# Kernel tuning notes

Hardware: AMD Instinct MI355X
Metric: run time of the kernel (lower is better)

## Reference

```python
import jax, jax.numpy as jnp
import numpy as np

EMBED_DIM = 1024
N_HEADS = 16
HEAD_DIM = EMBED_DIM // N_HEADS


def setup_inputs() -> dict:
    key = jax.random.key(0)
    k_x, k_wqkv, k_bqkv, k_wo, k_bo = jax.random.split(key, 5)
    s = 1.0 / np.sqrt(EMBED_DIM)
    return {
        "x": jax.random.normal(k_x, (2, 2048, EMBED_DIM), dtype=jnp.float32),
        "w_qkv": jax.random.uniform(k_wqkv, (EMBED_DIM, 3 * EMBED_DIM), jnp.float32, -s, s),
        "b_qkv": jax.random.uniform(k_bqkv, (3 * EMBED_DIM,), jnp.float32, -s, s),
        "w_out": jax.random.uniform(k_wo, (EMBED_DIM, EMBED_DIM), jnp.float32, -s, s),
        "b_out": jax.random.uniform(k_bo, (EMBED_DIM,), jnp.float32, -s, s),
    }


def reference(x, w_qkv, b_qkv, w_out, b_out):
    B, T, C = x.shape
    qkv = x @ w_qkv + b_qkv                      # [B,T,3C]
    q, k, v = jnp.split(qkv, 3, axis=-1)
    # [B,T,C] -> [B,H,T,D]
    def heads(t):
        return t.reshape(B, T, N_HEADS, HEAD_DIM).transpose(0, 2, 1, 3)
    q, k, v = heads(q), heads(k), heads(v)
    scale = 1.0 / np.sqrt(HEAD_DIM).astype(np.float32)
    scores = jnp.einsum("bhqd,bhkd->bhqk", q, k) * scale
    causal = jnp.tril(jnp.ones((T, T), dtype=bool))  # True where allowed
    scores = jnp.where(causal, scores, jnp.finfo(scores.dtype).min)
    attn = jax.nn.softmax(scores, axis=-1)
    out = jnp.einsum("bhqk,bhkd->bhqd", attn, v)
    out = out.transpose(0, 2, 1, 3).reshape(B, T, C)
    return out @ w_out + b_out
```

## Files before the change

kernel.cpp:

```cpp
#include <hip/hip_runtime.h>
#include <hip/hip_bf16.h>

typedef __attribute__((ext_vector_type(4))) float f32x4;
typedef __attribute__((ext_vector_type(8))) short bf16x8;

static __device__ __forceinline__ unsigned short f2bf(float f) {
  union { float f; unsigned u; } v;
  v.f = f;
  unsigned r = v.u + 0x7FFFu + ((v.u >> 16) & 1u);
  return (unsigned short)(r >> 16);
}

static __device__ __forceinline__ unsigned cvt_pk_bf16(float lo, float hi) {
  unsigned r;
  asm("v_cvt_pk_bf16_f32 %0, %1, %2" : "=v"(r) : "v"(lo), "v"(hi));
  return r;
}

static __device__ __forceinline__ void gload16(const void* g, void* lds) {
  __builtin_amdgcn_global_load_lds(
      (const __attribute__((address_space(1))) unsigned int*)g,
      (__attribute__((address_space(3))) unsigned int*)lds, 16, 0, 0);
}

__global__ __launch_bounds__(256) void prep_kernel(
    const float* __restrict__ x, const float* __restrict__ w_qkv,
    const float* __restrict__ w_out, unsigned short* __restrict__ xb,
    unsigned short* __restrict__ wqkvT, unsigned short* __restrict__ woT) {
  __shared__ float tile[32][33];
  const int bid = blockIdx.x, tid = threadIdx.x;
  if (bid < 4096) {
    int i = bid * 256 + tid;
    float4 v = reinterpret_cast<const float4*>(x)[i];
    ushort4 o;
    o.x = f2bf(v.x); o.y = f2bf(v.y); o.z = f2bf(v.z); o.w = f2bf(v.w);
    reinterpret_cast<ushort4*>(xb)[i] = o;
    return;
  }
  const float* src; unsigned short* dst; int c0, r0, C;
  if (bid < 7168) {
    int t = bid - 4096;
    src = w_qkv; dst = wqkvT; C = 3072;
    c0 = (t % 96) * 32; r0 = (t / 96) * 32;
  } else {
    int t = bid - 7168;
    src = w_out; dst = woT; C = 1024;
    c0 = (t & 31) * 32; r0 = (t >> 5) * 32;
  }
  int tx = tid & 31, ty = tid >> 5;
#pragma unroll
  for (int i = 0; i < 32; i += 8)
    tile[ty + i][tx] = src[(size_t)(r0 + ty + i) * C + c0 + tx];
  __syncthreads();
#pragma unroll
  for (int i = 0; i < 32; i += 8)
    dst[(size_t)(c0 + ty + i) * 1024 + r0 + tx] = f2bf(tile[tx][ty + i]);
}

template <int MODE, int BN>
__global__ __launch_bounds__(256, MODE == 0 ? 3 : 2) void gemm_bf16(
    const unsigned short* __restrict__ A,
    const unsigned short* __restrict__ Bt,
    const float* __restrict__ bias,
    unsigned short* __restrict__ q_out,
    unsigned short* __restrict__ k_out,
    unsigned short* __restrict__ v_out,
    float* __restrict__ f_out) {
  constexpr int NB2 = BN / 32;
  constexpr int NBL = BN / 64;
  __shared__ __align__(16) unsigned short As[2][128 * 32];
  __shared__ __align__(16) unsigned short Bs[2][BN * 32];

  const int tid = threadIdx.x;
  const int wid = tid >> 6, lane = tid & 63;
  const int l15 = lane & 15, g = lane >> 4;
  const int wm = wid >> 1, wn = wid & 1;
  const int n0 = blockIdx.x * BN, m0 = blockIdx.y * 128;

  f32x4 acc[4][NB2] = {};

  auto stage = [&](int k0, int bsel) {
#pragma unroll
    for (int i = 0; i < 2; ++i) {
      int t = tid + i * 256;
      int row = t >> 2, c8 = (t & 3) << 3;
      gload16(A + (size_t)(m0 + row) * 1024 + k0 + c8, &As[bsel][(i * 256 + wid * 64) * 8]);
    }
#pragma unroll
    for (int i = 0; i < NBL; ++i) {
      int t = tid + i * 256;
      int row = t >> 2, c8 = (t & 3) << 3;
      gload16(Bt + (size_t)(n0 + row) * 1024 + k0 + c8, &Bs[bsel][(i * 256 + wid * 64) * 8]);
    }
  };

  stage(0, 0);
  __syncthreads();
  for (int ks = 0; ks < 32; ++ks) {
    const int cur = ks & 1;
    if (ks + 1 < 32) stage((ks + 1) * 32, cur ^ 1);
    bf16x8 a[4], b[NB2];
#pragma unroll
    for (int mi = 0; mi < 4; ++mi)
      a[mi] = *reinterpret_cast<const bf16x8*>(&As[cur][(wm * 64 + mi * 16 + l15) * 32 + g * 8]);
#pragma unroll
    for (int ni = 0; ni < NB2; ++ni)
      b[ni] = *reinterpret_cast<const bf16x8*>(&Bs[cur][(wn * (BN / 2) + ni * 16 + l15) * 32 + g * 8]);
    __builtin_amdgcn_s_setprio(1);
#pragma unroll
    for (int mi = 0; mi < 4; ++mi)
#pragma unroll
      for (int ni = 0; ni < NB2; ++ni)
        acc[mi][ni] = __builtin_amdgcn_mfma_f32_16x16x32_bf16(a[mi], b[ni], acc[mi][ni], 0, 0, 0);
    __builtin_amdgcn_s_setprio(0);
    __syncthreads();
  }

  if (MODE == 0) {
    const int which = n0 >> 10;
    unsigned short* dst = (which == 0) ? q_out : (which == 1) ? k_out : v_out;
    const float oscale = (which == 0) ? 0.125f * 1.44269504f : 1.0f;
#pragma unroll
    for (int ni = 0; ni < NB2; ++ni) {
      int col = n0 + wn * (BN / 2) + ni * 16 + l15;
      int c = col & 1023;
      int h = c >> 6, d = c & 63;
      float bv = bias[col];
#pragma unroll
      for (int mi = 0; mi < 4; ++mi) {
#pragma unroll
        for (int r = 0; r < 4; ++r) {
          int rowg = m0 + wm * 64 + mi * 16 + g * 4 + r;
          int bb = rowg >> 11, tt = rowg & 2047;
          dst[((bb * 16 + h) * 2048 + tt) * 64 + d] = f2bf((acc[mi][ni][r] + bv) * oscale);
        }
      }
    }
  } else {
#pragma unroll
    for (int ni = 0; ni < NB2; ++ni) {
      int col = n0 + wn * (BN / 2) + ni * 16 + l15;
      float bv = bias[col];
#pragma unroll
      for (int mi = 0; mi < 4; ++mi)
#pragma unroll
        for (int r = 0; r < 4; ++r) {
          int rowg = m0 + wm * 64 + mi * 16 + g * 4 + r;
          f_out[(size_t)rowg * 1024 + col] = acc[mi][ni][r] + bv;
        }
    }
  }
}

#define KS_SZ (64 * 64)
#define VT_SZ (64 * 72)

__device__ __forceinline__ void attn_stage_K(const unsigned short* __restrict__ Kb,
                                             int k0, unsigned short* KsBuf,
                                             int tid, int wid) {
#pragma unroll
  for (int i = 0; i < 2; ++i) {
    int t = tid + i * 256;
    int row = t >> 3;
    int cb = (t & 7) << 4;
    int src = cb ^ ((row & 7) << 4);
    gload16((const char*)Kb + (size_t)(k0 + row) * 128 + src,
            (char*)KsBuf + (i * 256 + wid * 64) * 16);
  }
}

__device__ __forceinline__ void write_vt(unsigned short* VtBuf, int kvL, int d8,
                                         uint4 v0, uint4 v1) {
  unsigned* base = reinterpret_cast<unsigned*>(&VtBuf[(size_t)d8 * 72 + kvL]);
  unsigned lo, hi;
  lo = __builtin_amdgcn_perm(v1.x, v0.x, 0x05040100u);
  hi = __builtin_amdgcn_perm(v1.x, v0.x, 0x07060302u);
  base[0] = lo;   base[36] = hi;
  lo = __builtin_amdgcn_perm(v1.y, v0.y, 0x05040100u);
  hi = __builtin_amdgcn_perm(v1.y, v0.y, 0x07060302u);
  base[72] = lo;  base[108] = hi;
  lo = __builtin_amdgcn_perm(v1.z, v0.z, 0x05040100u);
  hi = __builtin_amdgcn_perm(v1.z, v0.z, 0x07060302u);
  base[144] = lo; base[180] = hi;
  lo = __builtin_amdgcn_perm(v1.w, v0.w, 0x05040100u);
  hi = __builtin_amdgcn_perm(v1.w, v0.w, 0x07060302u);
  base[216] = lo; base[252] = hi;
}

__device__ __forceinline__ void attn_run_qtile(
    const unsigned short* __restrict__ Qb,
    const unsigned short* __restrict__ Kb,
    const unsigned short* __restrict__ Vb,
    unsigned short* __restrict__ O,
    int b, int h, int q0, int nt,
    unsigned short* Ks, unsigned short* Vt, unsigned short* Ps,
    int tid, int wid, int l15, int g) {
  bf16x8 qf[2];
  {
    const unsigned short* qrow_p = Qb + (size_t)(q0 + wid * 16 + l15) * 64;
    qf[0] = *reinterpret_cast<const bf16x8*>(qrow_p + g * 8);
    qf[1] = *reinterpret_cast<const bf16x8*>(qrow_p + 32 + g * 8);
  }

  float m_run = -1e30f;
  float l_run = 0.0f;
  f32x4 ot[4] = {};
  const int qg = q0 + wid * 16 + l15;
  const int kvL = (tid & 31) * 2, d8 = (tid >> 5) * 8;
  const int qrow = wid * 16 + l15;

  attn_stage_K(Kb, 0, Ks, tid, wid);
  {
    const uint4* vp = reinterpret_cast<const uint4*>(Vb + (size_t)kvL * 64 + d8);
    write_vt(Vt, kvL, d8, vp[0], vp[8]);
  }
  __syncthreads();

  for (int t = 0; t < nt; ++t) {
    const unsigned short* KsC = Ks + (t & 1) * KS_SZ;
    const unsigned short* VtC = Vt + (t & 1) * VT_SZ;
    uint4 va, vb;
    const bool pf = (t + 1 < nt);
    if (pf) {
      attn_stage_K(Kb, (t + 1) << 6, Ks + ((t + 1) & 1) * KS_SZ, tid, wid);
      const uint4* vp = reinterpret_cast<const uint4*>(
          Vb + (size_t)(((t + 1) << 6) + kvL) * 64 + d8);
      va = vp[0];
      vb = vp[8];
    }

    f32x4 s[4] = {};
    __builtin_amdgcn_s_setprio(1);
#pragma unroll
    for (int kk = 0; kk < 2; ++kk)
#pragma unroll
      for (int mi = 0; mi < 4; ++mi) {
        int row = mi * 16 + l15;
        int cb = (kk * 64 + g * 16) ^ ((row & 7) << 4);
        bf16x8 kf = *reinterpret_cast<const bf16x8*>((const char*)KsC + row * 128 + cb);
        s[mi] = __builtin_amdgcn_mfma_f32_16x16x32_bf16(kf, qf[kk], s[mi], 0, 0, 0);
      }
    __builtin_amdgcn_s_setprio(0);

    if (t == nt - 1) {
      const int k0 = t << 6;
#pragma unroll
      for (int mi = 0; mi < 4; ++mi)
#pragma unroll
        for (int r = 0; r < 4; ++r) {
          int kvg = k0 + mi * 16 + g * 4 + r;
          s[mi][r] = (kvg <= qg) ? s[mi][r] : -1e30f;
        }
    }

    float pmax = -1e30f;
#pragma unroll
    for (int mi = 0; mi < 4; ++mi)
#pragma unroll
      for (int r = 0; r < 4; ++r) pmax = fmaxf(pmax, s[mi][r]);

    if (!__all(pmax <= m_run + 8.0f)) {
      float tmax = fmaxf(pmax, __shfl_xor(pmax, 16));
      tmax = fmaxf(tmax, __shfl_xor(tmax, 32));
      float m_new = fmaxf(m_run, tmax);
      float corr = __builtin_amdgcn_exp2f(m_run - m_new);
      l_run *= corr;
#pragma unroll
      for (int mi = 0; mi < 4; ++mi)
#pragma unroll
        for (int r = 0; r < 4; ++r) ot[mi][r] *= corr;
      m_run = m_new;
    }

    float tsum = 0.f;
#pragma unroll
    for (int mi = 0; mi < 4; ++mi) {
      float p0 = __builtin_amdgcn_exp2f(s[mi][0] - m_run);
      float p1 = __builtin_amdgcn_exp2f(s[mi][1] - m_run);
      float p2 = __builtin_amdgcn_exp2f(s[mi][2] - m_run);
      float p3 = __builtin_amdgcn_exp2f(s[mi][3] - m_run);
      tsum += (p0 + p1) + (p2 + p3);
      uint2 pk;
      pk.x = cvt_pk_bf16(p0, p1);
      pk.y = cvt_pk_bf16(p2, p3);
      *reinterpret_cast<uint2*>((char*)Ps + qrow * 144 + mi * 32 + g * 8) = pk;
    }
    l_run += tsum;

    __builtin_amdgcn_s_setprio(1);
#pragma unroll
    for (int kk = 0; kk < 2; ++kk) {
      bf16x8 pfr = *reinterpret_cast<const bf16x8*>(Ps + qrow * 72 + kk * 32 + g * 8);
#pragma unroll
      for (int mi = 0; mi < 4; ++mi) {
        bf16x8 vf = *reinterpret_cast<const bf16x8*>(VtC + (mi * 16 + l15) * 72 + kk * 32 + g * 8);
        ot[mi] = __builtin_amdgcn_mfma_f32_16x16x32_bf16(vf, pfr, ot[mi], 0, 0, 0);
      }
    }
    __builtin_amdgcn_s_setprio(0);

    if (pf) write_vt(Vt + ((t + 1) & 1) * VT_SZ, kvL, d8, va, vb);
    __syncthreads();
  }

  float l_tot = l_run + __shfl_xor(l_run, 16);
  l_tot += __shfl_xor(l_tot, 32);
  float inv_l = 1.0f / l_tot;

#pragma unroll
  for (int mi = 0; mi < 4; ++mi) {
    uint2 pk;
    pk.x = cvt_pk_bf16(ot[mi][0] * inv_l, ot[mi][1] * inv_l);
    pk.y = cvt_pk_bf16(ot[mi][2] * inv_l, ot[mi][3] * inv_l);
    int b0 = (mi * 32 + g * 8) ^ ((qrow & 7) << 4);
    *reinterpret_cast<uint2*>((char*)Ks + qrow * 128 + b0) = pk;
  }
  __syncthreads();
#pragma unroll
  for (int i = 0; i < 2; ++i) {
    int t = tid + i * 256;
    int row = t >> 3;
    int cb = (t & 7) << 4;
    int sw = cb ^ ((row & 7) << 4);
    bf16x8 vv = *reinterpret_cast<const bf16x8*>((const char*)Ks + row * 128 + sw);
    *reinterpret_cast<bf16x8*>(O + ((size_t)(b * 2048 + q0 + row)) * 1024 + h * 64 + (cb >> 1)) = vv;
  }
  __syncthreads();
}

__global__ __launch_bounds__(256, 2) void attn_fwd(
    const unsigned short* __restrict__ Q,
    const unsigned short* __restrict__ K,
    const unsigned short* __restrict__ V,
    unsigned short* __restrict__ O) {
  __shared__ __align__(16) unsigned short Ks[2 * KS_SZ];
  __shared__ __align__(16) unsigned short Vt[2 * VT_SZ];
  __shared__ __align__(16) unsigned short Ps[64 * 72];

  const int tid = threadIdx.x;
  const int wid = tid >> 6;
  const int l15 = tid & 15;
  const int g = (tid & 63) >> 4;

  int lin = blockIdx.x + (blockIdx.y << 4);
  int w = ((lin & 7) << 6) + (lin >> 3);
  const int pi = w & 15, bh = w >> 4;
  const int b = bh >> 4, h = bh & 15;

  const unsigned short* Qb = Q + (size_t)bh * 2048 * 64;
  const unsigned short* Kb = K + (size_t)bh * 2048 * 64;
  const unsigned short* Vb = V + (size_t)bh * 2048 * 64;

  attn_run_qtile(Qb, Kb, Vb, O, b, h, pi << 6, pi + 1, Ks, Vt, Ps, tid, wid, l15, g);
  attn_run_qtile(Qb, Kb, Vb, O, b, h, (31 - pi) << 6, 32 - pi, Ks, Vt, Ps, tid, wid, l15, g);
}

extern "C" void kernel_launch(void* const* d_in, const int* in_sizes, int n_in,
                              void* d_out, int out_size, void* d_ws, size_t ws_size,
                              hipStream_t stream) {
  const float* x = (const float*)d_in[0];
  const float* w_qkv = (const float*)d_in[1];
  const float* b_qkv = (const float*)d_in[2];
  const float* w_out = (const float*)d_in[3];
  const float* b_out = (const float*)d_in[4];
  float* out = (float*)d_out;
  char* ws = (char*)d_ws;

  unsigned short* xb    = (unsigned short*)d_out;
  unsigned short* wqkvT = (unsigned short*)(ws);
  unsigned short* woT   = (unsigned short*)(ws + 6291456);
  unsigned short* q_buf = (unsigned short*)(ws + 8388608);
  unsigned short* k_buf = (unsigned short*)(ws + 16777216);
  unsigned short* v_buf = (unsigned short*)(ws + 25165824);
  unsigned short* aout  = (unsigned short*)(ws + 33554432);

  prep_kernel<<<dim3(8192), dim3(256), 0, stream>>>(x, w_qkv, w_out, xb, wqkvT, woT);

  gemm_bf16<0, 128><<<dim3(24, 32), dim3(256), 0, stream>>>(
      xb, wqkvT, b_qkv, q_buf, k_buf, v_buf, nullptr);

  attn_fwd<<<dim3(16, 32), dim3(256), 0, stream>>>(q_buf, k_buf, v_buf, aout);

  gemm_bf16<1, 64><<<dim3(16, 32), dim3(256), 0, stream>>>(
      aout, woT, b_out, nullptr, nullptr, nullptr, out);
}
```

Measured before the change: 107.0 us.

## Process paired causal query tiles together in one KV pass

The attention kernel now runs both paired query tiles (short tile pi and long tile 31-pi) in a single loop over KV tiles. Each staged K/V tile is loaded once and shared by both, instead of the short tile's KV range being streamed twice. K and V fragments are hoisted into registers and reused by both MFMA chains, and the P buffer is doubled. The block-index mapping also changes to a 1D grid ordered by pair index. This raises register and LDS pressure and may reduce occupancy.

Result: no change. 108.6 us (+1.5%).

```diff
diff --git a/kernel.cpp b/kernel.cpp
--- a/kernel.cpp
+++ b/kernel.cpp
@@ -187,147 +187,6 @@
   base[216] = lo; base[252] = hi;
 }
 
-__device__ __forceinline__ void attn_run_qtile(
-    const unsigned short* __restrict__ Qb,
-    const unsigned short* __restrict__ Kb,
-    const unsigned short* __restrict__ Vb,
-    unsigned short* __restrict__ O,
-    int b, int h, int q0, int nt,
-    unsigned short* Ks, unsigned short* Vt, unsigned short* Ps,
-    int tid, int wid, int l15, int g) {
-  bf16x8 qf[2];
-  {
-    const unsigned short* qrow_p = Qb + (size_t)(q0 + wid * 16 + l15) * 64;
-    qf[0] = *reinterpret_cast<const bf16x8*>(qrow_p + g * 8);
-    qf[1] = *reinterpret_cast<const bf16x8*>(qrow_p + 32 + g * 8);
-  }
-
-  float m_run = -1e30f;
-  float l_run = 0.0f;
-  f32x4 ot[4] = {};
-  const int qg = q0 + wid * 16 + l15;
-  const int kvL = (tid & 31) * 2, d8 = (tid >> 5) * 8;
-  const int qrow = wid * 16 + l15;
-
-  attn_stage_K(Kb, 0, Ks, tid, wid);
-  {
-    const uint4* vp = reinterpret_cast<const uint4*>(Vb + (size_t)kvL * 64 + d8);
-    write_vt(Vt, kvL, d8, vp[0], vp[8]);
-  }
-  __syncthreads();
-
-  for (int t = 0; t < nt; ++t) {
-    const unsigned short* KsC = Ks + (t & 1) * KS_SZ;
-    const unsigned short* VtC = Vt + (t & 1) * VT_SZ;
-    uint4 va, vb;
-    const bool pf = (t + 1 < nt);
-    if (pf) {
-      attn_stage_K(Kb, (t + 1) << 6, Ks + ((t + 1) & 1) * KS_SZ, tid, wid);
-      const uint4* vp = reinterpret_cast<const uint4*>(
-          Vb + (size_t)(((t + 1) << 6) + kvL) * 64 + d8);
-      va = vp[0];
-      vb = vp[8];
-    }
-
-    f32x4 s[4] = {};
-    __builtin_amdgcn_s_setprio(1);
-#pragma unroll
-    for (int kk = 0; kk < 2; ++kk)
-#pragma unroll
-      for (int mi = 0; mi < 4; ++mi) {
-        int row = mi * 16 + l15;
-        int cb = (kk * 64 + g * 16) ^ ((row & 7) << 4);
-        bf16x8 kf = *reinterpret_cast<const bf16x8*>((const char*)KsC + row * 128 + cb);
-        s[mi] = __builtin_amdgcn_mfma_f32_16x16x32_bf16(kf, qf[kk], s[mi], 0, 0, 0);
-      }
-    __builtin_amdgcn_s_setprio(0);
-
-    if (t == nt - 1) {
-      const int k0 = t << 6;
-#pragma unroll
-      for (int mi = 0; mi < 4; ++mi)
-#pragma unroll
-        for (int r = 0; r < 4; ++r) {
-          int kvg = k0 + mi * 16 + g * 4 + r;
-          s[mi][r] = (kvg <= qg) ? s[mi][r] : -1e30f;
-        }
-    }
-
-    float pmax = -1e30f;
-#pragma unroll
-    for (int mi = 0; mi < 4; ++mi)
-#pragma unroll
-      for (int r = 0; r < 4; ++r) pmax = fmaxf(pmax, s[mi][r]);
-
-    if (!__all(pmax <= m_run + 8.0f)) {
-      float tmax = fmaxf(pmax, __shfl_xor(pmax, 16));
-      tmax = fmaxf(tmax, __shfl_xor(tmax, 32));
-      float m_new = fmaxf(m_run, tmax);
-      float corr = __builtin_amdgcn_exp2f(m_run - m_new);
-      l_run *= corr;
-#pragma unroll
-      for (int mi = 0; mi < 4; ++mi)
-#pragma unroll
-        for (int r = 0; r < 4; ++r) ot[mi][r] *= corr;
-      m_run = m_new;
-    }
-
-    float tsum = 0.f;
-#pragma unroll
-    for (int mi = 0; mi < 4; ++mi) {
-      float p0 = __builtin_amdgcn_exp2f(s[mi][0] - m_run);
-      float p1 = __builtin_amdgcn_exp2f(s[mi][1] - m_run);
-      float p2 = __builtin_amdgcn_exp2f(s[mi][2] - m_run);
-      float p3 = __builtin_amdgcn_exp2f(s[mi][3] - m_run);
-      tsum += (p0 + p1) + (p2 + p3);
-      uint2 pk;
-      pk.x = cvt_pk_bf16(p0, p1);
-      pk.y = cvt_pk_bf16(p2, p3);
-      *reinterpret_cast<uint2*>((char*)Ps + qrow * 144 + mi * 32 + g * 8) = pk;
-    }
-    l_run += tsum;
-
-    __builtin_amdgcn_s_setprio(1);
-#pragma unroll
-    for (int kk = 0; kk < 2; ++kk) {
-      bf16x8 pfr = *reinterpret_cast<const bf16x8*>(Ps + qrow * 72 + kk * 32 + g * 8);
-#pragma unroll
-      for (int mi = 0; mi < 4; ++mi) {
-        bf16x8 vf = *reinterpret_cast<const bf16x8*>(VtC + (mi * 16 + l15) * 72 + kk * 32 + g * 8);
-        ot[mi] = __builtin_amdgcn_mfma_f32_16x16x32_bf16(vf, pfr, ot[mi], 0, 0, 0);
-      }
-    }
-    __builtin_amdgcn_s_setprio(0);
-
-    if (pf) write_vt(Vt + ((t + 1) & 1) * VT_SZ, kvL, d8, va, vb);
-    __syncthreads();
-  }
-
-  float l_tot = l_run + __shfl_xor(l_run, 16);
-  l_tot += __shfl_xor(l_tot, 32);
-  float inv_l = 1.0f / l_tot;
-
-#pragma unroll
-  for (int mi = 0; mi < 4; ++mi) {
-    uint2 pk;
-    pk.x = cvt_pk_bf16(ot[mi][0] * inv_l, ot[mi][1] * inv_l);
-    pk.y = cvt_pk_bf16(ot[mi][2] * inv_l, ot[mi][3] * inv_l);
-    int b0 = (mi * 32 + g * 8) ^ ((qrow & 7) << 4);
-    *reinterpret_cast<uint2*>((char*)Ks + qrow * 128 + b0) = pk;
-  }
-  __syncthreads();
-#pragma unroll
-  for (int i = 0; i < 2; ++i) {
-    int t = tid + i * 256;
-    int row = t >> 3;
-    int cb = (t & 7) << 4;
-    int sw = cb ^ ((row & 7) << 4);
-    bf16x8 vv = *reinterpret_cast<const bf16x8*>((const char*)Ks + row * 128 + sw);
-    *reinterpret_cast<bf16x8*>(O + ((size_t)(b * 2048 + q0 + row)) * 1024 + h * 64 + (cb >> 1)) = vv;
-  }
-  __syncthreads();
-}
-
 __global__ __launch_bounds__(256, 2) void attn_fwd(
     const unsigned short* __restrict__ Q,
     const unsigned short* __restrict__ K,
@@ -335,24 +194,246 @@
     unsigned short* __restrict__ O) {
   __shared__ __align__(16) unsigned short Ks[2 * KS_SZ];
   __shared__ __align__(16) unsigned short Vt[2 * VT_SZ];
-  __shared__ __align__(16) unsigned short Ps[64 * 72];
+  __shared__ __align__(16) unsigned short Ps[2 * 64 * 72];
 
   const int tid = threadIdx.x;
   const int wid = tid >> 6;
   const int l15 = tid & 15;
   const int g = (tid & 63) >> 4;
 
-  int lin = blockIdx.x + (blockIdx.y << 4);
-  int w = ((lin & 7) << 6) + (lin >> 3);
-  const int pi = w & 15, bh = w >> 4;
+  const int lin = blockIdx.x;
+  const int pi = lin >> 5, bh = lin & 31;
   const int b = bh >> 4, h = bh & 15;
+  const int q0A = pi << 6, q0B = (31 - pi) << 6;
+  const int nB = 32 - pi;
 
   const unsigned short* Qb = Q + (size_t)bh * 2048 * 64;
   const unsigned short* Kb = K + (size_t)bh * 2048 * 64;
   const unsigned short* Vb = V + (size_t)bh * 2048 * 64;
 
-  attn_run_qtile(Qb, Kb, Vb, O, b, h, pi << 6, pi + 1, Ks, Vt, Ps, tid, wid, l15, g);
-  attn_run_qtile(Qb, Kb, Vb, O, b, h, (31 - pi) << 6, 32 - pi, Ks, Vt, Ps, tid, wid, l15, g);
+  bf16x8 qfA[2], qfB[2];
+  {
+    const unsigned short* qa = Qb + (size_t)(q0A + wid * 16 + l15) * 64;
+    qfA[0] = *reinterpret_cast<const bf16x8*>(qa + g * 8);
+    qfA[1] = *reinterpret_cast<const bf16x8*>(qa + 32 + g * 8);
+    const unsigned short* qb2 = Qb + (size_t)(q0B + wid * 16 + l15) * 64;
+    qfB[0] = *reinterpret_cast<const bf16x8*>(qb2 + g * 8);
+    qfB[1] = *reinterpret_cast<const bf16x8*>(qb2 + 32 + g * 8);
+  }
+
+  float mA = -1e30f, lA = 0.f, mB = -1e30f, lB = 0.f;
+  f32x4 otA[4] = {}, otB[4] = {};
+  const int qgA = q0A + wid * 16 + l15;
+  const int qgB = q0B + wid * 16 + l15;
+  const int kvL = (tid & 31) * 2, d8 = (tid >> 5) * 8;
+  const int qrow = wid * 16 + l15;
+  unsigned short* PsA = Ps;
+  unsigned short* PsB = Ps + 64 * 72;
+
+  attn_stage_K(Kb, 0, Ks, tid, wid);
+  {
+    const uint4* vp = reinterpret_cast<const uint4*>(Vb + (size_t)kvL * 64 + d8);
+    write_vt(Vt, kvL, d8, vp[0], vp[8]);
+  }
+  __syncthreads();
+
+  for (int t = 0; t < nB; ++t) {
+    const unsigned short* KsC = Ks + (t & 1) * KS_SZ;
+    const unsigned short* VtC = Vt + (t & 1) * VT_SZ;
+    uint4 va, vb;
+    const bool pf = (t + 1 < nB);
+    const bool hasA = (t <= pi);
+    if (pf) {
+      attn_stage_K(Kb, (t + 1) << 6, Ks + ((t + 1) & 1) * KS_SZ, tid, wid);
+      const uint4* vp = reinterpret_cast<const uint4*>(
+          Vb + (size_t)(((t + 1) << 6) + kvL) * 64 + d8);
+      va = vp[0];
+      vb = vp[8];
+    }
+
+    bf16x8 kf[2][4];
+#pragma unroll
+    for (int kk = 0; kk < 2; ++kk)
+#pragma unroll
+      for (int mi = 0; mi < 4; ++mi) {
+        int row = mi * 16 + l15;
+        int cb = (kk * 64 + g * 16) ^ ((row & 7) << 4);
+        kf[kk][mi] = *reinterpret_cast<const bf16x8*>((const char*)KsC + row * 128 + cb);
+      }
+
+    f32x4 sB[4] = {};
+    __builtin_amdgcn_s_setprio(1);
+#pragma unroll
+    for (int kk = 0; kk < 2; ++kk)
+#pragma unroll
+      for (int mi = 0; mi < 4; ++mi)
+        sB[mi] = __builtin_amdgcn_mfma_f32_16x16x32_bf16(kf[kk][mi], qfB[kk], sB[mi], 0, 0, 0);
+    __builtin_amdgcn_s_setprio(0);
+    f32x4 sA[4] = {};
+    if (hasA) {
+      __builtin_amdgcn_s_setprio(1);
+#pragma unroll
+      for (int kk = 0; kk < 2; ++kk)
+#pragma unroll
+        for (int mi = 0; mi < 4; ++mi)
+          sA[mi] = __builtin_amdgcn_mfma_f32_16x16x32_bf16(kf[kk][mi], qfA[kk], sA[mi], 0, 0, 0);
+      __builtin_amdgcn_s_setprio(0);
+    }
+
+    if (t == nB - 1) {
+      const int k0 = t << 6;
+#pragma unroll
+      for (int mi = 0; mi < 4; ++mi)
+#pragma unroll
+        for (int r = 0; r < 4; ++r) {
+          int kvg = k0 + mi * 16 + g * 4 + r;
+          sB[mi][r] = (kvg <= qgB) ? sB[mi][r] : -1e30f;
+        }
+    }
+    {
+      float pmax = -1e30f;
+#pragma unroll
+      for (int mi = 0; mi < 4; ++mi)
+#pragma unroll
+        for (int r = 0; r < 4; ++r) pmax = fmaxf(pmax, sB[mi][r]);
+      if (!__all(pmax <= mB + 8.0f)) {
+        float tmax = fmaxf(pmax, __shfl_xor(pmax, 16));
+        tmax = fmaxf(tmax, __shfl_xor(tmax, 32));
+        float m_new = fmaxf(mB, tmax);
+        float corr = __builtin_amdgcn_exp2f(mB - m_new);
+        lB *= corr;
+#pragma unroll
+        for (int mi = 0; mi < 4; ++mi)
+#pragma unroll
+          for (int r = 0; r < 4; ++r) otB[mi][r] *= corr;
+        mB = m_new;
+      }
+      float tsum = 0.f;
+#pragma unroll
+      for (int mi = 0; mi < 4; ++mi) {
+        float p0 = __builtin_amdgcn_exp2f(sB[mi][0] - mB);
+        float p1 = __builtin_amdgcn_exp2f(sB[mi][1] - mB);
+        float p2 = __builtin_amdgcn_exp2f(sB[mi][2] - mB);
+        float p3 = __builtin_amdgcn_exp2f(sB[mi][3] - mB);
+        tsum += (p0 + p1) + (p2 + p3);
+        uint2 pk;
+        pk.x = cvt_pk_bf16(p0, p1);
+        pk.y = cvt_pk_bf16(p2, p3);
+        *reinterpret_cast<uint2*>((char*)PsB + qrow * 144 + mi * 32 + g * 8) = pk;
+      }
+      lB += tsum;
+    }
+
+    bf16x8 vf[2][4];
+#pragma unroll
+    for (int kk = 0; kk < 2; ++kk)
+#pragma unroll
+      for (int mi = 0; mi < 4; ++mi)
+        vf[kk][mi] = *reinterpret_cast<const bf16x8*>(VtC + (mi * 16 + l15) * 72 + kk * 32 + g * 8);
+
+    if (hasA) {
+      if (t == pi) {
+        const int k0 = t << 6;
+#pragma unroll
+        for (int mi = 0; mi < 4; ++mi)
+#pragma unroll
+          for (int r = 0; r < 4; ++r) {
+            int kvg = k0 + mi * 16 + g * 4 + r;
+            sA[mi][r] = (kvg <= qgA) ? sA[mi][r] : -1e30f;
+          }
+      }
+      float pmax = -1e30f;
+#pragma unroll
+      for (int mi = 0; mi < 4; ++mi)
+#pragma unroll
+        for (int r = 0; r < 4; ++r) pmax = fmaxf(pmax, sA[mi][r]);
+      if (!__all(pmax <= mA + 8.0f)) {
+        float tmax = fmaxf(pmax, __shfl_xor(pmax, 16));
+        tmax = fmaxf(tmax, __shfl_xor(tmax, 32));
+        float m_new = fmaxf(mA, tmax);
+        float corr = __builtin_amdgcn_exp2f(mA - m_new);
+        lA *= corr;
+#pragma unroll
+        for (int mi = 0; mi < 4; ++mi)
+#pragma unroll
+          for (int r = 0; r < 4; ++r) otA[mi][r] *= corr;
+        mA = m_new;
+      }
+      float tsum = 0.f;
+#pragma unroll
+      for (int mi = 0; mi < 4; ++mi) {
+        float p0 = __builtin_amdgcn_exp2f(sA[mi][0] - mA);
+        float p1 = __builtin_amdgcn_exp2f(sA[mi][1] - mA);
+        float p2 = __builtin_amdgcn_exp2f(sA[mi][2] - mA);
+        float p3 = __builtin_amdgcn_exp2f(sA[mi][3] - mA);
+        tsum += (p0 + p1) + (p2 + p3);
+        uint2 pk;
+        pk.x = cvt_pk_bf16(p0, p1);
+        pk.y = cvt_pk_bf16(p2, p3);
+        *reinterpret_cast<uint2*>((char*)PsA + qrow * 144 + mi * 32 + g * 8) = pk;
+      }
+      lA += tsum;
+    }
+
+    {
+      bf16x8 pfrB[2];
+      pfrB[0] = *reinterpret_cast<const bf16x8*>(PsB + qrow * 72 + g * 8);
+      pfrB[1] = *reinterpret_cast<const bf16x8*>(PsB + qrow * 72 + 32 + g * 8);
+      __builtin_amdgcn_s_setprio(1);
+#pragma unroll
+      for (int kk = 0; kk < 2; ++kk)
+#pragma unroll
+        for (int mi = 0; mi < 4; ++mi)
+          otB[mi] = __builtin_amdgcn_mfma_f32_16x16x32_bf16(vf[kk][mi], pfrB[kk], otB[mi], 0, 0, 0);
+      __builtin_amdgcn_s_setprio(0);
+    }
+    if (hasA) {
+      bf16x8 pfrA[2];
+      pfrA[0] = *reinterpret_cast<const bf16x8*>(PsA + qrow * 72 + g * 8);
+      pfrA[1] = *reinterpret_cast<const bf16x8*>(PsA + qrow * 72 + 32 + g * 8);
+      __builtin_amdgcn_s_setprio(1);
+#pragma unroll
+      for (int kk = 0; kk < 2; ++kk)
+#pragma unroll
+        for (int mi = 0; mi < 4; ++mi)
+          otA[mi] = __builtin_amdgcn_mfma_f32_16x16x32_bf16(vf[kk][mi], pfrA[kk], otA[mi], 0, 0, 0);
+      __builtin_amdgcn_s_setprio(0);
+    }
+
+    if (pf) write_vt(Vt + ((t + 1) & 1) * VT_SZ, kvL, d8, va, vb);
+    __syncthreads();
+  }
+
+  float ltA = lA + __shfl_xor(lA, 16);
+  ltA += __shfl_xor(ltA, 32);
+  float invA = 1.0f / ltA;
+  float ltB = lB + __shfl_xor(lB, 16);
+  ltB += __shfl_xor(ltB, 32);
+  float invB = 1.0f / ltB;
+
+#pragma unroll
+  for (int mi = 0; mi < 4; ++mi) {
+    uint2 pkA, pkB;
+    pkA.x = cvt_pk_bf16(otA[mi][0] * invA, otA[mi][1] * invA);
+    pkA.y = cvt_pk_bf16(otA[mi][2] * invA, otA[mi][3] * invA);
+    pkB.x = cvt_pk_bf16(otB[mi][0] * invB, otB[mi][1] * invB);
+    pkB.y = cvt_pk_bf16(otB[mi][2] * invB, otB[mi][3] * invB);
+    int b0 = (mi * 32 + g * 8) ^ ((qrow & 7) << 4);
+    *reinterpret_cast<uint2*>((char*)Ks + qrow * 128 + b0) = pkA;
+    *reinterpret_cast<uint2*>((char*)Vt + qrow * 128 + b0) = pkB;
+  }
+  __syncthreads();
+#pragma unroll
+  for (int i = 0; i < 2; ++i) {
+    int t = tid + i * 256;
+    int row = t >> 3;
+    int cb = (t & 7) << 4;
+    int sw = cb ^ ((row & 7) << 4);
+    bf16x8 vA = *reinterpret_cast<const bf16x8*>((const char*)Ks + row * 128 + sw);
+    bf16x8 vB = *reinterpret_cast<const bf16x8*>((const char*)Vt + row * 128 + sw);
+    *reinterpret_cast<bf16x8*>(O + ((size_t)(b * 2048 + q0A + row)) * 1024 + h * 64 + (cb >> 1)) = vA;
+    *reinterpret_cast<bf16x8*>(O + ((size_t)(b * 2048 + q0B + row)) * 1024 + h * 64 + (cb >> 1)) = vB;
+  }
 }
 
 extern "C" void kernel_launch(void* const* d_in, const int* in_sizes, int n_in,
@@ -379,7 +460,7 @@
   gemm_bf16<0, 128><<<dim3(24, 32), dim3(256), 0, stream>>>(
       xb, wqkvT, b_qkv, q_buf, k_buf, v_buf, nullptr);
 
-  attn_fwd<<<dim3(16, 32), dim3(256), 0, stream>>>(q_buf, k_buf, v_buf, aout);
+  attn_fwd<<<dim3(512), dim3(256), 0, stream>>>(q_buf, k_buf, v_buf, aout);
 
   gemm_bf16<1, 64><<<dim3(16, 32), dim3(256), 0, stream>>>(
       aout, woT, b_out, nullptr, nullptr, nullptr, out);
```

## Split attention into one q-tile per block with XOR-swizzled LDS layout

Applied to the files above, without the earlier changes.

The attention kernel now runs one 64-row query tile per block over 1024 blocks, instead of pairing a short and a long tile in each of 512 blocks. Blocks are ordered longest-first so the causal workload balances better. The V-transpose and P buffers drop their 72-element padding for a 64-wide XOR-swizzled layout, which shrinks LDS use, and launch bounds are raised to 4 blocks per CU for higher occupancy. The cost is more launched blocks, each paying its own prologue and epilogue, and possible register pressure under the tighter launch bound.

New measurement: 107.2 us. About the same (+0.2%).

```diff
diff --git a/kernel.cpp b/kernel.cpp
--- a/kernel.cpp
+++ b/kernel.cpp
@@ -153,7 +153,7 @@
 }
 
 #define KS_SZ (64 * 64)
-#define VT_SZ (64 * 72)
+#define VT_SZ (64 * 64)
 
 __device__ __forceinline__ void attn_stage_K(const unsigned short* __restrict__ Kb,
                                              int k0, unsigned short* KsBuf,
@@ -171,30 +171,52 @@
 
 __device__ __forceinline__ void write_vt(unsigned short* VtBuf, int kvL, int d8,
                                          uint4 v0, uint4 v1) {
-  unsigned* base = reinterpret_cast<unsigned*>(&VtBuf[(size_t)d8 * 72 + kvL]);
+  char* base = (char*)VtBuf + (size_t)d8 * 128;
+  const int c = kvL * 2;
   unsigned lo, hi;
   lo = __builtin_amdgcn_perm(v1.x, v0.x, 0x05040100u);
   hi = __builtin_amdgcn_perm(v1.x, v0.x, 0x07060302u);
-  base[0] = lo;   base[36] = hi;
+  *reinterpret_cast<unsigned*>(base + 0 * 128 + (c ^ (0 << 4))) = lo;
+  *reinterpret_cast<unsigned*>(base + 1 * 128 + (c ^ (1 << 4))) = hi;
   lo = __builtin_amdgcn_perm(v1.y, v0.y, 0x05040100u);
   hi = __builtin_amdgcn_perm(v1.y, v0.y, 0x07060302u);
-  base[72] = lo;  base[108] = hi;
+  *reinterpret_cast<unsigned*>(base + 2 * 128 + (c ^ (2 << 4))) = lo;
+  *reinterpret_cast<unsigned*>(base + 3 * 128 + (c ^ (3 << 4))) = hi;
   lo = __builtin_amdgcn_perm(v1.z, v0.z, 0x05040100u);
   hi = __builtin_amdgcn_perm(v1.z, v0.z, 0x07060302u);
-  base[144] = lo; base[180] = hi;
+  *reinterpret_cast<unsigned*>(base + 4 * 128 + (c ^ (4 << 4))) = lo;
+  *reinterpret_cast<unsigned*>(base + 5 * 128 + (c ^ (5 << 4))) = hi;
   lo = __builtin_amdgcn_perm(v1.w, v0.w, 0x05040100u);
   hi = __builtin_amdgcn_perm(v1.w, v0.w, 0x07060302u);
-  base[216] = lo; base[252] = hi;
-}
-
-__device__ __forceinline__ void attn_run_qtile(
-    const unsigned short* __restrict__ Qb,
-    const unsigned short* __restrict__ Kb,
-    const unsigned short* __restrict__ Vb,
-    unsigned short* __restrict__ O,
-    int b, int h, int q0, int nt,
-    unsigned short* Ks, unsigned short* Vt, unsigned short* Ps,
-    int tid, int wid, int l15, int g) {
+  *reinterpret_cast<unsigned*>(base + 6 * 128 + (c ^ (6 << 4))) = lo;
+  *reinterpret_cast<unsigned*>(base + 7 * 128 + (c ^ (7 << 4))) = hi;
+}
+
+__global__ __launch_bounds__(256, 4) void attn_fwd(
+    const unsigned short* __restrict__ Q,
+    const unsigned short* __restrict__ K,
+    const unsigned short* __restrict__ V,
+    unsigned short* __restrict__ O) {
+  __shared__ __align__(16) unsigned short Ks[2 * KS_SZ];
+  __shared__ __align__(16) unsigned short Vt[2 * VT_SZ];
+  __shared__ __align__(16) unsigned short Ps[64 * 64];
+
+  const int tid = threadIdx.x;
+  const int wid = tid >> 6;
+  const int l15 = tid & 15;
+  const int g = (tid & 63) >> 4;
+
+  const int lin = blockIdx.x;
+  const int bh = lin & 31;
+  const int o = lin >> 5, oq = o & 7, os = o >> 3;
+  const int qt = (os == 0) ? 31 - oq : (os == 1) ? 16 + oq : (os == 2) ? 15 - oq : oq;
+  const int b = bh >> 4, h = bh & 15;
+  const int q0 = qt << 6, nt = qt + 1;
+
+  const unsigned short* Qb = Q + (size_t)bh * 2048 * 64;
+  const unsigned short* Kb = K + (size_t)bh * 2048 * 64;
+  const unsigned short* Vb = V + (size_t)bh * 2048 * 64;
+
   bf16x8 qf[2];
   {
     const unsigned short* qrow_p = Qb + (size_t)(q0 + wid * 16 + l15) * 64;
@@ -208,6 +230,7 @@
   const int qg = q0 + wid * 16 + l15;
   const int kvL = (tid & 31) * 2, d8 = (tid >> 5) * 8;
   const int qrow = wid * 16 + l15;
+  const int sP = (qrow & 7) << 4;
 
   attn_stage_K(Kb, 0, Ks, tid, wid);
   {
@@ -283,17 +306,20 @@
       uint2 pk;
       pk.x = cvt_pk_bf16(p0, p1);
       pk.y = cvt_pk_bf16(p2, p3);
-      *reinterpret_cast<uint2*>((char*)Ps + qrow * 144 + mi * 32 + g * 8) = pk;
+      *reinterpret_cast<uint2*>((char*)Ps + qrow * 128 + ((mi * 32 + g * 8) ^ sP)) = pk;
     }
     l_run += tsum;
 
     __builtin_amdgcn_s_setprio(1);
 #pragma unroll
     for (int kk = 0; kk < 2; ++kk) {
-      bf16x8 pfr = *reinterpret_cast<const bf16x8*>(Ps + qrow * 72 + kk * 32 + g * 8);
+      bf16x8 pfr = *reinterpret_cast<const bf16x8*>(
+          (const char*)Ps + qrow * 128 + ((kk * 64 + g * 16) ^ sP));
 #pragma unroll
       for (int mi = 0; mi < 4; ++mi) {
-        bf16x8 vf = *reinterpret_cast<const bf16x8*>(VtC + (mi * 16 + l15) * 72 + kk * 32 + g * 8);
+        int row = mi * 16 + l15;
+        bf16x8 vf = *reinterpret_cast<const bf16x8*>(
+            (const char*)VtC + row * 128 + ((kk * 64 + g * 16) ^ ((row & 7) << 4)));
         ot[mi] = __builtin_amdgcn_mfma_f32_16x16x32_bf16(vf, pfr, ot[mi], 0, 0, 0);
       }
     }
@@ -312,7 +338,7 @@
     uint2 pk;
     pk.x = cvt_pk_bf16(ot[mi][0] * inv_l, ot[mi][1] * inv_l);
     pk.y = cvt_pk_bf16(ot[mi][2] * inv_l, ot[mi][3] * inv_l);
-    int b0 = (mi * 32 + g * 8) ^ ((qrow & 7) << 4);
+    int b0 = (mi * 32 + g * 8) ^ sP;
     *reinterpret_cast<uint2*>((char*)Ks + qrow * 128 + b0) = pk;
   }
   __syncthreads();
@@ -325,34 +351,6 @@
     bf16x8 vv = *reinterpret_cast<const bf16x8*>((const char*)Ks + row * 128 + sw);
     *reinterpret_cast<bf16x8*>(O + ((size_t)(b * 2048 + q0 + row)) * 1024 + h * 64 + (cb >> 1)) = vv;
   }
-  __syncthreads();
-}
-
-__global__ __launch_bounds__(256, 2) void attn_fwd(
-    const unsigned short* __restrict__ Q,
-    const unsigned short* __restrict__ K,
-    const unsigned short* __restrict__ V,
-    unsigned short* __restrict__ O) {
-  __shared__ __align__(16) unsigned short Ks[2 * KS_SZ];
-  __shared__ __align__(16) unsigned short Vt[2 * VT_SZ];
-  __shared__ __align__(16) unsigned short Ps[64 * 72];
-
-  const int tid = threadIdx.x;
-  const int wid = tid >> 6;
-  const int l15 = tid & 15;
-  const int g = (tid & 63) >> 4;
-
-  int lin = blockIdx.x + (blockIdx.y << 4);
-  int w = ((lin & 7) << 6) + (lin >> 3);
-  const int pi = w & 15, bh = w >> 4;
-  const int b = bh >> 4, h = bh & 15;
-
-  const unsigned short* Qb = Q + (size_t)bh * 2048 * 64;
-  const unsigned short* Kb = K + (size_t)bh * 2048 * 64;
-  const unsigned short* Vb = V + (size_t)bh * 2048 * 64;
-
-  attn_run_qtile(Qb, Kb, Vb, O, b, h, pi << 6, pi + 1, Ks, Vt, Ps, tid, wid, l15, g);
-  attn_run_qtile(Qb, Kb, Vb, O, b, h, (31 - pi) << 6, 32 - pi, Ks, Vt, Ps, tid, wid, l15, g);
 }
 
 extern "C" void kernel_launch(void* const* d_in, const int* in_sizes, int n_in,
@@ -379,7 +377,7 @@
   gemm_bf16<0, 128><<<dim3(24, 32), dim3(256), 0, stream>>>(
       xb, wqkvT, b_qkv, q_buf, k_buf, v_buf, nullptr);
 
-  attn_fwd<<<dim3(16, 32), dim3(256), 0, stream>>>(q_buf, k_buf, v_buf, aout);
+  attn_fwd<<<dim3(1024), dim3(256), 0, stream>>>(q_buf, k_buf, v_buf, aout);
 
   gemm_bf16<1, 64><<<dim3(16, 32), dim3(256), 0, stream>>>(
       aout, woT, b_out, nullptr, nullptr, nullptr, out);
```
